# Kernel optimization log

Measured on AMD Instinct MI355X. Metric: run time of the kernel, lower is better.

## Reference

```python
import jax, jax.numpy as jnp
import numpy as np

B, N, L = 1, 512, 384
D_IN, D_OUT, HEADS, D_FF = 128, 64, 4, 256
EPS = 1e-5


def layer_norm(x, g, b):
    m = jnp.mean(x, axis=-1, keepdims=True)
    v = jnp.mean((x - m) ** 2, axis=-1, keepdims=True)
    return g * (x - m) / jnp.sqrt(v + EPS) + b


def setup_inputs() -> dict:
    key = jax.random.key(0)
    ks = jax.random.split(key, 10)
    s = 0.05
    return {
        "src": jax.random.normal(ks[0], (B, L, L, D_IN), jnp.float32),
        "tgt": jax.random.normal(ks[1], (B, N, L, D_OUT), jnp.float32),
        "Wp": jax.random.normal(ks[2], (D_IN, HEADS), jnp.float32) * s,
        "bp": jnp.zeros((HEADS,), jnp.float32),
        "Wm": jax.random.normal(ks[3], (D_OUT, D_OUT), jnp.float32) * s,
        "bm": jnp.zeros((D_OUT,), jnp.float32),
        "Wo": jax.random.normal(ks[4], (D_OUT, D_OUT), jnp.float32) * s,
        "bo": jnp.zeros((D_OUT,), jnp.float32),
        "W1": jax.random.normal(ks[5], (D_OUT, D_FF), jnp.float32) * s,
        "b1": jnp.zeros((D_FF,), jnp.float32),
        "W2": jax.random.normal(ks[6], (D_FF, D_OUT), jnp.float32) * s,
        "b2": jnp.zeros((D_OUT,), jnp.float32),
        "g_norm": jnp.ones((D_IN,), jnp.float32),
        "bt_norm": jnp.zeros((D_IN,), jnp.float32),
        "g1": jnp.ones((D_OUT,), jnp.float32),
        "bt1": jnp.zeros((D_OUT,), jnp.float32),
        "g2": jnp.ones((D_OUT,), jnp.float32),
        "bt2": jnp.zeros((D_OUT,), jnp.float32),
    }


def reference(src, tgt, Wp, bp, Wm, bm, Wo, bo, W1, b1, W2, b2,
              g_norm, bt_norm, g1, bt1, g2, bt2):
    H = HEADS
    C = D_OUT // H  # channels per head group
    # symmetrize pair features over the two residue axes
    src = 0.5 * (src + jnp.swapaxes(src, 1, 2))
    src = layer_norm(src, g_norm, bt_norm)
    tgt2 = layer_norm(tgt, g1, bt1)
    # attention map from pair features; softmax over the FIRST residue axis (dim=1)
    attn = jax.nn.softmax(src @ Wp + bp, axis=1)          # [B, L(k), L(l), H]
    # value projection of MSA, split channels into (C, H) matching view(B,-1,H,N,L)
    v = (tgt2 @ Wm + bm).reshape(B, N, L, C, H)           # [B, N, L(k), C, H]
    # out[b,n,l,c,h] = sum_k v[b,n,k,c,h] * attn[b,k,l,h]
    o = jnp.einsum('bnkch,bklh->bnlch', v, attn).reshape(B, N, L, D_OUT)
    tgt2 = o @ Wo + bo
    tgt = tgt + tgt2
    # norm2 (view to (B*N,L,-1) is irrelevant: LN acts on last dim) + FFN
    tgt2 = layer_norm(tgt, g2, bt2)
    tgt2 = jax.nn.relu(tgt2 @ W1 + b1) @ W2 + b2
    return tgt + tgt2
```

## Files before the change

### kernel.cpp

```cpp
#include <hip/hip_runtime.h>
#include <math.h>

#define LL 384
#define NN 512
#define DIN 128
#define DOUT 64
#define HH 4
#define CC 16
#define DFF 256
#define EPS 1e-5f

typedef __attribute__((ext_vector_type(4))) float f32x4;
typedef __attribute__((ext_vector_type(8))) short bf16x8;

__device__ __forceinline__ short f2bf(float f) {
    union { float f; unsigned u; } v; v.f = f;
    unsigned r = v.u + 0x7fff + ((v.u >> 16) & 1);
    return (short)(r >> 16);
}
#define MFMA16(a, b, c) __builtin_amdgcn_mfma_f32_16x16x32_bf16(a, b, c, 0, 0, 0)

__global__ __launch_bounds__(256) void k1_logits(
    const float* __restrict__ src, const float* __restrict__ Wp,
    const float* __restrict__ bp, const float* __restrict__ g_norm,
    const float* __restrict__ bt_norm, float* __restrict__ logits)
{
    int k = blockIdx.x;
    int wave = threadIdx.x >> 6;
    int lane = threadIdx.x & 63;
    int l = blockIdx.y * 4 + wave;
    if (k > l) return;
    const float* r1 = src + ((size_t)k * LL + l) * DIN;
    const float* r2 = src + ((size_t)l * LL + k) * DIN;
    float2 a = *(const float2*)(r1 + lane * 2);
    float2 b = *(const float2*)(r2 + lane * 2);
    float x0 = 0.5f * (a.x + b.x);
    float x1 = 0.5f * (a.y + b.y);
    float s = x0 + x1, ss = x0 * x0 + x1 * x1;
    #pragma unroll
    for (int m = 1; m < 64; m <<= 1) { s += __shfl_xor(s, m); ss += __shfl_xor(ss, m); }
    float mean = s * (1.0f / DIN);
    float var  = ss * (1.0f / DIN) - mean * mean;
    float rstd = rsqrtf(var + EPS);
    int d0 = lane * 2;
    float n0 = g_norm[d0]     * (x0 - mean) * rstd + bt_norm[d0];
    float n1 = g_norm[d0 + 1] * (x1 - mean) * rstd + bt_norm[d0 + 1];
    float4 w0 = *(const float4*)(Wp + d0 * HH);
    float4 w1 = *(const float4*)(Wp + d0 * HH + HH);
    float p0 = n0 * w0.x + n1 * w1.x;
    float p1 = n0 * w0.y + n1 * w1.y;
    float p2 = n0 * w0.z + n1 * w1.z;
    float p3 = n0 * w0.w + n1 * w1.w;
    #pragma unroll
    for (int m = 1; m < 64; m <<= 1) {
        p0 += __shfl_xor(p0, m); p1 += __shfl_xor(p1, m);
        p2 += __shfl_xor(p2, m); p3 += __shfl_xor(p3, m);
    }
    int hh = lane & 3;
    float pv = (hh == 0 ? p0 : hh == 1 ? p1 : hh == 2 ? p2 : p3) + bp[hh];
    if (lane < 4)                 logits[((size_t)l * HH + hh) * LL + k] = pv;
    else if (lane < 8 && k != l)  logits[((size_t)k * HH + hh) * LL + l] = pv;
}

__global__ __launch_bounds__(256) void k2_softmax(
    const float* __restrict__ logits, short* __restrict__ attn_bf)
{
    int l = blockIdx.x;
    int h = threadIdx.x >> 6;
    int lane = threadIdx.x & 63;
    const float* row = logits + ((size_t)l * HH + h) * LL;
    float v[6];
    float mx = -1e30f;
    #pragma unroll
    for (int j = 0; j < 6; j++) { v[j] = row[lane + 64 * j]; mx = fmaxf(mx, v[j]); }
    #pragma unroll
    for (int m = 1; m < 64; m <<= 1) mx = fmaxf(mx, __shfl_xor(mx, m));
    float sum = 0.f;
    #pragma unroll
    for (int j = 0; j < 6; j++) { v[j] = __expf(v[j] - mx); sum += v[j]; }
    #pragma unroll
    for (int m = 1; m < 64; m <<= 1) sum += __shfl_xor(sum, m);
    float inv = 1.0f / sum;
    short* orow = attn_bf + ((size_t)h * LL + l) * LL;
    #pragma unroll
    for (int j = 0; j < 6; j++) orow[lane + 64 * j] = f2bf(v[j] * inv);
}

__global__ __launch_bounds__(256) void k3_v(
    const float* __restrict__ tgt, const float* __restrict__ Wm,
    const float* __restrict__ bm, const float* __restrict__ g1,
    const float* __restrict__ bt1, short* __restrict__ vt_bf)
{
    int tid = threadIdx.x, wave = tid >> 6, lane = tid & 63;
    int c15 = lane & 15, g = lane >> 4;
    bf16x8 wb[2][4];
    #pragma unroll
    for (int kf = 0; kf < 2; kf++)
        #pragma unroll
        for (int nt = 0; nt < 4; nt++) {
            bf16x8 w;
            #pragma unroll
            for (int i = 0; i < 8; i++) {
                int k = kf * 32 + g * 8 + i;
                w[i] = f2bf(Wm[k * DOUT + c15 * HH + nt]);
            }
            wb[kf][nt] = w;
        }
    float bmr[4];
    #pragma unroll
    for (int nt = 0; nt < 4; nt++) bmr[nt] = bm[c15 * HH + nt];
    float g1a[8], g1b[8], bta[8], btb[8];
    #pragma unroll
    for (int i = 0; i < 8; i++) {
        g1a[i] = g1[g * 8 + i];       bta[i] = bt1[g * 8 + i];
        g1b[i] = g1[32 + g * 8 + i];  btb[i] = bt1[32 + g * 8 + i];
    }
    const f32x4 zero = {0.f, 0.f, 0.f, 0.f};
    int gwave = blockIdx.x * 4 + wave;
    int nwaves = gridDim.x * 4;
    const int NT = NN * LL / 16;
    for (int t = gwave; t < NT; t += nwaves) {
        int r0 = t * 16;
        const float* tb = tgt + (size_t)r0 * DOUT + c15 * DOUT + g * 8;
        float4 xa = *(const float4*)(tb);
        float4 xb = *(const float4*)(tb + 4);
        float4 xc = *(const float4*)(tb + 32);
        float4 xd = *(const float4*)(tb + 36);
        float ya[8] = {xa.x, xa.y, xa.z, xa.w, xb.x, xb.y, xb.z, xb.w};
        float yb[8] = {xc.x, xc.y, xc.z, xc.w, xd.x, xd.y, xd.z, xd.w};
        float s = 0.f, ss = 0.f;
        #pragma unroll
        for (int i = 0; i < 8; i++) {
            s += ya[i] + yb[i];
            ss += ya[i] * ya[i] + yb[i] * yb[i];
        }
        s  += __shfl_xor(s, 16);  s  += __shfl_xor(s, 32);
        ss += __shfl_xor(ss, 16); ss += __shfl_xor(ss, 32);
        float mean = s * (1.0f / DOUT);
        float var  = ss * (1.0f / DOUT) - mean * mean;
        float rstd = rsqrtf(var + EPS);
        bf16x8 a0, a1;
        #pragma unroll
        for (int i = 0; i < 8; i++) {
            a0[i] = f2bf(g1a[i] * (ya[i] - mean) * rstd + bta[i]);
            a1[i] = f2bf(g1b[i] * (yb[i] - mean) * rstd + btb[i]);
        }
        f32x4 acc[4];
        #pragma unroll
        for (int nt = 0; nt < 4; nt++) {
            acc[nt] = MFMA16(a0, wb[0][nt], zero);
            acc[nt] = MFMA16(a1, wb[1][nt], acc[nt]);
        }
        int n = r0 / LL, k0 = r0 % LL;
        #pragma unroll
        for (int nt = 0; nt < 4; nt++)
            #pragma unroll
            for (int j = 0; j < 4; j++) {
                int k = k0 + g * 4 + j;
                vt_bf[((size_t)(nt * LL + k)) * (NN * CC) + n * CC + c15] =
                    f2bf(acc[nt][j] + bmr[nt]);
            }
    }
}

#define K4S 56
__global__ __launch_bounds__(256) void k4_mfma(
    const short* __restrict__ attn_bf, const short* __restrict__ vt_bf,
    short* __restrict__ o_bf)
{
    __shared__ short As[LL * K4S];
    __shared__ short Bs[64 * K4S];
    int h = blockIdx.y;
    int m0 = blockIdx.x * 64;
    int tid = threadIdx.x, wave = tid >> 6, lane = tid & 63;
    int c15 = lane & 15, g = lane >> 4;
    f32x4 acc[6][4];
    #pragma unroll
    for (int i = 0; i < 6; i++)
        #pragma unroll
        for (int nt = 0; nt < 4; nt++) acc[i][nt] = (f32x4){0.f, 0.f, 0.f, 0.f};

    for (int k0 = 0; k0 < LL; k0 += 32) {
        __syncthreads();
        #pragma unroll
        for (int it = 0; it < 6; it++) {
            int e = tid + 256 * it;
            int l = e >> 2, k8 = (e & 3) * 8;
            bf16x8 v = *(const bf16x8*)(attn_bf + ((size_t)(h * LL + l)) * LL + k0 + k8);
            *(bf16x8*)(As + l * K4S + k8) = v;
        }
        {
            int m = tid & 63, kg = tid >> 6;
            const short* vb = vt_bf + ((size_t)(h * LL + k0 + kg * 8)) * (NN * CC) + m0 + m;
            short tmp[8];
            #pragma unroll
            for (int j = 0; j < 8; j++) tmp[j] = vb[(size_t)j * (NN * CC)];
            #pragma unroll
            for (int j = 0; j < 4; j++) {
                int v2 = (int)(unsigned short)tmp[2 * j] | ((int)(unsigned short)tmp[2 * j + 1] << 16);
                *(int*)(Bs + m * K4S + kg * 8 + 2 * j) = v2;
            }
        }
        __syncthreads();
        bf16x8 bfr[4];
        #pragma unroll
        for (int nt = 0; nt < 4; nt++)
            bfr[nt] = *(const bf16x8*)(Bs + (nt * 16 + c15) * K4S + g * 8);
        #pragma unroll
        for (int i = 0; i < 6; i++) {
            int l = (wave + 4 * i) * 16 + c15;
            bf16x8 afr = *(const bf16x8*)(As + l * K4S + g * 8);
            #pragma unroll
            for (int nt = 0; nt < 4; nt++)
                acc[i][nt] = MFMA16(afr, bfr[nt], acc[i][nt]);
        }
    }
    #pragma unroll
    for (int i = 0; i < 6; i++) {
        int l = (wave + 4 * i) * 16 + g * 4;
        #pragma unroll
        for (int nt = 0; nt < 4; nt++) {
            int n = (m0 >> 4) + nt;
            #pragma unroll
            for (int r = 0; r < 4; r++)
                o_bf[((size_t)n * LL + l + r) * DOUT + h * 16 + c15] = f2bf(acc[i][nt][r]);
        }
    }
}

#define W1TS 72
#define W2TS 264
#define K5_LDS ((DFF * W1TS + DOUT * W2TS + 8 * 16 * W2TS) * 2)
__global__ __launch_bounds__(512) void k5_tail(
    const short* __restrict__ o_bf, const float* __restrict__ tgt,
    const float* __restrict__ Wo, const float* __restrict__ bo,
    const float* __restrict__ W1, const float* __restrict__ b1,
    const float* __restrict__ W2, const float* __restrict__ b2,
    const float* __restrict__ g2, const float* __restrict__ bt2,
    float* __restrict__ out)
{
    extern __shared__ short smem[];
    short* W1T = smem;
    short* W2T = W1T + DFF * W1TS;
    short* Fl  = W2T + DOUT * W2TS;
    int tid = threadIdx.x, wave = tid >> 6, lane = tid & 63;
    int c15 = lane & 15, g = lane >> 4;

    for (int e = tid; e < DOUT * DFF; e += 512) {
        int k = e >> 8, p = e & 255;
        W1T[p * W1TS + k] = f2bf(W1[e]);
        int k2 = e >> 6, n = e & 63;
        W2T[n * W2TS + k2] = f2bf(W2[e]);
    }
    bf16x8 woB[2][4];
    #pragma unroll
    for (int kf = 0; kf < 2; kf++)
        #pragma unroll
        for (int nt = 0; nt < 4; nt++) {
            bf16x8 w;
            #pragma unroll
            for (int i2 = 0; i2 < 8; i2++) {
                int k = kf * 32 + g * 8 + i2;
                int rj = (k & 15) * 4 + (k >> 4);
                w[i2] = f2bf(Wo[rj * DOUT + nt * 16 + c15]);
            }
            woB[kf][nt] = w;
        }
    float bor[4], b2r[4], g2r[4], bt2r[4], b1r[16];
    #pragma unroll
    for (int nt = 0; nt < 4; nt++) {
        bor[nt]  = bo[nt * 16 + c15];  b2r[nt]  = b2[nt * 16 + c15];
        g2r[nt]  = g2[nt * 16 + c15];  bt2r[nt] = bt2[nt * 16 + c15];
    }
    #pragma unroll
    for (int nt = 0; nt < 16; nt++) b1r[nt] = b1[nt * 16 + c15];
    __syncthreads();

    short* Fw = Fl + wave * 16 * W2TS;
    int gwave = blockIdx.x * 8 + wave;
    const f32x4 zero = {0.f, 0.f, 0.f, 0.f};

    for (int it = 0; it < 6; it++) {
        int r0 = (gwave * 6 + it) * 16;
        const short* ob = o_bf + (size_t)r0 * DOUT;
        bf16x8 oa0 = *(const bf16x8*)(ob + c15 * DOUT + g * 8);
        bf16x8 oa1 = *(const bf16x8*)(ob + c15 * DOUT + 32 + g * 8);
        f32x4 X[4];
        #pragma unroll
        for (int nt = 0; nt < 4; nt++) {
            X[nt] = MFMA16(oa0, woB[0][nt], zero);
            X[nt] = MFMA16(oa1, woB[1][nt], X[nt]);
        }
        const float* tb = tgt + (size_t)r0 * DOUT;
        #pragma unroll
        for (int nt = 0; nt < 4; nt++)
            #pragma unroll
            for (int j = 0; j < 4; j++)
                X[nt][j] += tb[(g * 4 + j) * DOUT + nt * 16 + c15] + bor[nt];
        #pragma unroll
        for (int j = 0; j < 4; j++) {
            float s  = X[0][j] + X[1][j] + X[2][j] + X[3][j];
            float ss = X[0][j]*X[0][j] + X[1][j]*X[1][j] + X[2][j]*X[2][j] + X[3][j]*X[3][j];
            #pragma unroll
            for (int m = 1; m < 16; m <<= 1) { s += __shfl_xor(s, m); ss += __shfl_xor(ss, m); }
            float mean = s * (1.0f / DOUT);
            float var  = ss * (1.0f / DOUT) - mean * mean;
            float rstd = rsqrtf(var + EPS);
            #pragma unroll
            for (int nt = 0; nt < 4; nt++) {
                float y = g2r[nt] * (X[nt][j] - mean) * rstd + bt2r[nt];
                Fw[(g * 4 + j) * W2TS + nt * 16 + c15] = f2bf(y);
            }
        }
        bf16x8 ya0 = *(const bf16x8*)(Fw + c15 * W2TS + g * 8);
        bf16x8 ya1 = *(const bf16x8*)(Fw + c15 * W2TS + 32 + g * 8);
        f32x4 Fa[16];
        #pragma unroll
        for (int nt = 0; nt < 16; nt++) {
            bf16x8 wb0 = *(const bf16x8*)(W1T + (nt * 16 + c15) * W1TS + g * 8);
            bf16x8 wb1 = *(const bf16x8*)(W1T + (nt * 16 + c15) * W1TS + 32 + g * 8);
            Fa[nt] = MFMA16(ya0, wb0, zero);
            Fa[nt] = MFMA16(ya1, wb1, Fa[nt]);
        }
        #pragma unroll
        for (int nt = 0; nt < 16; nt++)
            #pragma unroll
            for (int j = 0; j < 4; j++)
                Fw[(g * 4 + j) * W2TS + nt * 16 + c15] = f2bf(fmaxf(Fa[nt][j] + b1r[nt], 0.f));
        bf16x8 fa[8];
        #pragma unroll
        for (int kf = 0; kf < 8; kf++)
            fa[kf] = *(const bf16x8*)(Fw + c15 * W2TS + kf * 32 + g * 8);
        #pragma unroll
        for (int nt = 0; nt < 4; nt++)
            #pragma unroll
            for (int kf = 0; kf < 8; kf++) {
                bf16x8 wb = *(const bf16x8*)(W2T + (nt * 16 + c15) * W2TS + kf * 32 + g * 8);
                X[nt] = MFMA16(fa[kf], wb, X[nt]);
            }
        float* outb = out + (size_t)r0 * DOUT;
        #pragma unroll
        for (int nt = 0; nt < 4; nt++)
            #pragma unroll
            for (int j = 0; j < 4; j++)
                outb[(g * 4 + j) * DOUT + nt * 16 + c15] = X[nt][j] + b2r[nt];
    }
}

extern "C" void kernel_launch(void* const* d_in, const int* in_sizes, int n_in,
                              void* d_out, int out_size, void* d_ws, size_t ws_size,
                              hipStream_t stream)
{
    (void)in_sizes; (void)n_in; (void)out_size; (void)ws_size;
    const float* src     = (const float*)d_in[0];
    const float* tgt     = (const float*)d_in[1];
    const float* Wp      = (const float*)d_in[2];
    const float* bp      = (const float*)d_in[3];
    const float* Wm      = (const float*)d_in[4];
    const float* bm      = (const float*)d_in[5];
    const float* Wo      = (const float*)d_in[6];
    const float* bo      = (const float*)d_in[7];
    const float* W1      = (const float*)d_in[8];
    const float* b1      = (const float*)d_in[9];
    const float* W2      = (const float*)d_in[10];
    const float* b2      = (const float*)d_in[11];
    const float* g_norm  = (const float*)d_in[12];
    const float* bt_norm = (const float*)d_in[13];
    const float* g1      = (const float*)d_in[14];
    const float* bt1     = (const float*)d_in[15];
    const float* g2      = (const float*)d_in[16];
    const float* bt2     = (const float*)d_in[17];
    float* out = (float*)d_out;
    float* ws  = (float*)d_ws;

    float* logits  = ws;
    short* attn_bf = (short*)(ws + 589824);
    short* vt_bf   = attn_bf + 589824;
    short* o_bf    = vt_bf + 12582912;

    hipFuncSetAttribute((const void*)k5_tail,
                        hipFuncAttributeMaxDynamicSharedMemorySize, K5_LDS);

    k1_logits <<<dim3(LL, LL / 4), 256, 0, stream>>>(src, Wp, bp, g_norm, bt_norm, logits);
    k2_softmax<<<LL, 256, 0, stream>>>(logits, attn_bf);
    k3_v      <<<1024, 256, 0, stream>>>(tgt, Wm, bm, g1, bt1, vt_bf);
    k4_mfma   <<<dim3((NN * CC) / 64, HH), 256, 0, stream>>>(attn_bf, vt_bf, o_bf);
    k5_tail   <<<256, 512, K5_LDS, stream>>>(o_bf, tgt, Wo, bo, W1, b1, W2, b2, g2, bt2, out);
}
```

Measured before the change: 284.4 us.

## Process 32 rows per wave in FFN tail with swizzled LDS layout

The tail kernel now handles two 16-row tiles per iteration, so each W1/W2 fragment loaded from LDS feeds two MFMAs instead of one. The FFN hidden dimension is split into two chunks of 128 to bound register pressure and to shrink the per-wave staging buffer. An XOR swizzle on LDS columns aims to reduce bank conflicts, and launch bounds request two blocks per CU. The risk is higher register use per wave and larger LDS use per block, which could limit occupancy.

```diff
diff --git a/kernel.cpp b/kernel.cpp
--- a/kernel.cpp
+++ b/kernel.cpp
@@ -228,10 +228,12 @@
     }
 }
 
+#define SW(col, row) ((col) ^ ((((row) >> 2) & 3) << 4))
 #define W1TS 72
 #define W2TS 264
-#define K5_LDS ((DFF * W1TS + DOUT * W2TS + 8 * 16 * W2TS) * 2)
-__global__ __launch_bounds__(512) void k5_tail(
+#define FS 136
+#define K5_LDS ((DFF * W1TS + DOUT * W2TS + 8 * 32 * FS) * 2)
+__global__ __launch_bounds__(512, 2) void k5_tail(
     const short* __restrict__ o_bf, const float* __restrict__ tgt,
     const float* __restrict__ Wo, const float* __restrict__ bo,
     const float* __restrict__ W1, const float* __restrict__ b1,
@@ -248,9 +250,9 @@
 
     for (int e = tid; e < DOUT * DFF; e += 512) {
         int k = e >> 8, p = e & 255;
-        W1T[p * W1TS + k] = f2bf(W1[e]);
+        W1T[p * W1TS + SW(k, p)] = f2bf(W1[e]);
         int k2 = e >> 6, n = e & 63;
-        W2T[n * W2TS + k2] = f2bf(W2[e]);
+        W2T[n * W2TS + SW(k2, n)] = f2bf(W2[e]);
     }
     bf16x8 woB[2][4];
     #pragma unroll
@@ -273,77 +275,113 @@
         g2r[nt]  = g2[nt * 16 + c15];  bt2r[nt] = bt2[nt * 16 + c15];
     }
     #pragma unroll
-    for (int nt = 0; nt < 16; nt++) b1r[nt] = b1[nt * 16 + c15];
+    for (int pt = 0; pt < 16; pt++) b1r[pt] = b1[pt * 16 + c15];
     __syncthreads();
 
-    short* Fw = Fl + wave * 16 * W2TS;
+    short* Fw = Fl + wave * 32 * FS;
     int gwave = blockIdx.x * 8 + wave;
     const f32x4 zero = {0.f, 0.f, 0.f, 0.f};
 
-    for (int it = 0; it < 6; it++) {
-        int r0 = (gwave * 6 + it) * 16;
-        const short* ob = o_bf + (size_t)r0 * DOUT;
-        bf16x8 oa0 = *(const bf16x8*)(ob + c15 * DOUT + g * 8);
-        bf16x8 oa1 = *(const bf16x8*)(ob + c15 * DOUT + 32 + g * 8);
-        f32x4 X[4];
-        #pragma unroll
-        for (int nt = 0; nt < 4; nt++) {
-            X[nt] = MFMA16(oa0, woB[0][nt], zero);
-            X[nt] = MFMA16(oa1, woB[1][nt], X[nt]);
-        }
-        const float* tb = tgt + (size_t)r0 * DOUT;
-        #pragma unroll
-        for (int nt = 0; nt < 4; nt++)
-            #pragma unroll
-            for (int j = 0; j < 4; j++)
-                X[nt][j] += tb[(g * 4 + j) * DOUT + nt * 16 + c15] + bor[nt];
-        #pragma unroll
-        for (int j = 0; j < 4; j++) {
-            float s  = X[0][j] + X[1][j] + X[2][j] + X[3][j];
-            float ss = X[0][j]*X[0][j] + X[1][j]*X[1][j] + X[2][j]*X[2][j] + X[3][j]*X[3][j];
-            #pragma unroll
-            for (int m = 1; m < 16; m <<= 1) { s += __shfl_xor(s, m); ss += __shfl_xor(ss, m); }
-            float mean = s * (1.0f / DOUT);
-            float var  = ss * (1.0f / DOUT) - mean * mean;
-            float rstd = rsqrtf(var + EPS);
+    for (int it = 0; it < 3; it++) {
+        int r0 = (gwave * 3 + it) * 32;
+        f32x4 X[2][4];
+        #pragma unroll
+        for (int h = 0; h < 2; h++) {
+            const short* ob = o_bf + ((size_t)(r0 + h * 16) + c15) * DOUT;
+            bf16x8 oa0 = *(const bf16x8*)(ob + g * 8);
+            bf16x8 oa1 = *(const bf16x8*)(ob + 32 + g * 8);
             #pragma unroll
             for (int nt = 0; nt < 4; nt++) {
-                float y = g2r[nt] * (X[nt][j] - mean) * rstd + bt2r[nt];
-                Fw[(g * 4 + j) * W2TS + nt * 16 + c15] = f2bf(y);
-            }
-        }
-        bf16x8 ya0 = *(const bf16x8*)(Fw + c15 * W2TS + g * 8);
-        bf16x8 ya1 = *(const bf16x8*)(Fw + c15 * W2TS + 32 + g * 8);
-        f32x4 Fa[16];
-        #pragma unroll
-        for (int nt = 0; nt < 16; nt++) {
-            bf16x8 wb0 = *(const bf16x8*)(W1T + (nt * 16 + c15) * W1TS + g * 8);
-            bf16x8 wb1 = *(const bf16x8*)(W1T + (nt * 16 + c15) * W1TS + 32 + g * 8);
-            Fa[nt] = MFMA16(ya0, wb0, zero);
-            Fa[nt] = MFMA16(ya1, wb1, Fa[nt]);
-        }
-        #pragma unroll
-        for (int nt = 0; nt < 16; nt++)
-            #pragma unroll
-            for (int j = 0; j < 4; j++)
-                Fw[(g * 4 + j) * W2TS + nt * 16 + c15] = f2bf(fmaxf(Fa[nt][j] + b1r[nt], 0.f));
-        bf16x8 fa[8];
-        #pragma unroll
-        for (int kf = 0; kf < 8; kf++)
-            fa[kf] = *(const bf16x8*)(Fw + c15 * W2TS + kf * 32 + g * 8);
-        #pragma unroll
-        for (int nt = 0; nt < 4; nt++)
-            #pragma unroll
-            for (int kf = 0; kf < 8; kf++) {
-                bf16x8 wb = *(const bf16x8*)(W2T + (nt * 16 + c15) * W2TS + kf * 32 + g * 8);
-                X[nt] = MFMA16(fa[kf], wb, X[nt]);
-            }
-        float* outb = out + (size_t)r0 * DOUT;
-        #pragma unroll
-        for (int nt = 0; nt < 4; nt++)
-            #pragma unroll
-            for (int j = 0; j < 4; j++)
-                outb[(g * 4 + j) * DOUT + nt * 16 + c15] = X[nt][j] + b2r[nt];
+                X[h][nt] = MFMA16(oa0, woB[0][nt], zero);
+                X[h][nt] = MFMA16(oa1, woB[1][nt], X[h][nt]);
+            }
+            const float* tb = tgt + (size_t)(r0 + h * 16) * DOUT;
+            #pragma unroll
+            for (int nt = 0; nt < 4; nt++)
+                #pragma unroll
+                for (int j = 0; j < 4; j++)
+                    X[h][nt][j] += tb[(g * 4 + j) * DOUT + nt * 16 + c15] + bor[nt];
+        }
+        #pragma unroll
+        for (int h = 0; h < 2; h++)
+            #pragma unroll
+            for (int j = 0; j < 4; j++) {
+                float s  = X[h][0][j] + X[h][1][j] + X[h][2][j] + X[h][3][j];
+                float ss = X[h][0][j]*X[h][0][j] + X[h][1][j]*X[h][1][j]
+                         + X[h][2][j]*X[h][2][j] + X[h][3][j]*X[h][3][j];
+                #pragma unroll
+                for (int m = 1; m < 16; m <<= 1) { s += __shfl_xor(s, m); ss += __shfl_xor(ss, m); }
+                float mean = s * (1.0f / DOUT);
+                float var  = ss * (1.0f / DOUT) - mean * mean;
+                float rstd = rsqrtf(var + EPS);
+                int row = h * 16 + g * 4 + j;
+                #pragma unroll
+                for (int nt = 0; nt < 4; nt++) {
+                    float y = g2r[nt] * (X[h][nt][j] - mean) * rstd + bt2r[nt];
+                    Fw[row * FS + SW(nt * 16 + c15, row)] = f2bf(y);
+                }
+            }
+        bf16x8 ya0[2], ya1[2];
+        #pragma unroll
+        for (int h = 0; h < 2; h++) {
+            int yr = h * 16 + c15;
+            ya0[h] = *(const bf16x8*)(Fw + yr * FS + SW(g * 8, yr));
+            ya1[h] = *(const bf16x8*)(Fw + yr * FS + SW(32 + g * 8, yr));
+        }
+        #pragma unroll
+        for (int ch = 0; ch < 2; ch++) {
+            f32x4 Fa[2][8];
+            #pragma unroll
+            for (int nt8 = 0; nt8 < 8; nt8++) {
+                int pt = ch * 8 + nt8;
+                int wr = pt * 16 + c15;
+                bf16x8 w0 = *(const bf16x8*)(W1T + wr * W1TS + SW(g * 8, wr));
+                bf16x8 w1 = *(const bf16x8*)(W1T + wr * W1TS + SW(32 + g * 8, wr));
+                #pragma unroll
+                for (int h = 0; h < 2; h++) {
+                    Fa[h][nt8] = MFMA16(ya0[h], w0, zero);
+                    Fa[h][nt8] = MFMA16(ya1[h], w1, Fa[h][nt8]);
+                }
+            }
+            #pragma unroll
+            for (int h = 0; h < 2; h++)
+                #pragma unroll
+                for (int nt8 = 0; nt8 < 8; nt8++)
+                    #pragma unroll
+                    for (int j = 0; j < 4; j++) {
+                        int row = h * 16 + g * 4 + j;
+                        Fw[row * FS + SW(nt8 * 16 + c15, row)] =
+                            f2bf(fmaxf(Fa[h][nt8][j] + b1r[ch * 8 + nt8], 0.f));
+                    }
+            bf16x8 fa[2][4];
+            #pragma unroll
+            for (int h = 0; h < 2; h++) {
+                int fr = h * 16 + c15;
+                #pragma unroll
+                for (int kfl = 0; kfl < 4; kfl++)
+                    fa[h][kfl] = *(const bf16x8*)(Fw + fr * FS + SW(kfl * 32 + g * 8, fr));
+            }
+            #pragma unroll
+            for (int nt = 0; nt < 4; nt++) {
+                int wr2 = nt * 16 + c15;
+                #pragma unroll
+                for (int kfl = 0; kfl < 4; kfl++) {
+                    bf16x8 w = *(const bf16x8*)(W2T + wr2 * W2TS + SW((ch * 4 + kfl) * 32 + g * 8, wr2));
+                    #pragma unroll
+                    for (int h = 0; h < 2; h++)
+                        X[h][nt] = MFMA16(fa[h][kfl], w, X[h][nt]);
+                }
+            }
+        }
+        #pragma unroll
+        for (int h = 0; h < 2; h++) {
+            float* outb = out + (size_t)(r0 + h * 16) * DOUT;
+            #pragma unroll
+            for (int nt = 0; nt < 4; nt++)
+                #pragma unroll
+                for (int j = 0; j < 4; j++)
+                    outb[(g * 4 + j) * DOUT + nt * 16 + c15] = X[h][nt][j] + b2r[nt];
+        }
     }
 }
 
```

Result: slower. 300.7 us (+5.7%).
